# Performance work log

Measured on AMD Instinct MI355X. Metric: run time of the kernel, lower is better.

The kernel has to match this reference:

```python
import jax, jax.numpy as jnp
import numpy as np

N = 100000   # nodes
E = 1600000  # edges
DIM = 64
DIMS = [128, 64, 64, 64]  # [2*DIM] + 3*[DIM]
MAX_DEG = 64
NUM_LAB = 16

def _leaky(x):
    return jnp.where(x >= 0, x, 0.01 * x)

def _bn(x, g, b, eps=1e-5):
    # BatchNorm1d in training mode: per-feature batch mean / biased variance
    m = x.mean(axis=0)
    v = x.var(axis=0)
    return (x - m) * jax.lax.rsqrt(v + eps) * g + b

def setup_inputs() -> dict:
    key = jax.random.key(0)
    ks = jax.random.split(key, 40)
    d = {}
    d["node_deg"] = jax.random.randint(ks[0], (N,), 0, MAX_DEG + 1)
    d["node_lab"] = jax.random.randint(ks[1], (N,), 0, NUM_LAB)
    d["edge_index"] = jax.random.randint(ks[2], (2, E), 0, N)
    d["emb_deg"] = jax.random.normal(ks[3], (MAX_DEG + 1, DIM), jnp.float32) * 0.1
    d["emb_lab"] = jax.random.normal(ks[4], (NUM_LAB, DIM), jnp.float32) * 0.1
    k = 5
    for i, (n1, n2) in enumerate(zip(DIMS[:-1], DIMS[1:])):
        d[f"w{i}"] = jax.random.normal(ks[k], (n2, n1), jnp.float32) / np.sqrt(n1); k += 1
        d[f"b{i}"] = jnp.zeros((n2,), jnp.float32)
        d[f"g{i}"] = jnp.ones((n2,), jnp.float32)
        d[f"be{i}"] = jnp.zeros((n2,), jnp.float32)
    SUMD = sum(DIMS)  # 320
    d["fw1"] = jax.random.normal(ks[k], (DIM, SUMD), jnp.float32) / np.sqrt(SUMD); k += 1
    d["fb1"] = jnp.zeros((DIM,), jnp.float32)
    d["fg"] = jnp.ones((DIM,), jnp.float32)
    d["fbe"] = jnp.zeros((DIM,), jnp.float32)
    d["fw2"] = jax.random.normal(ks[k], (1, DIM), jnp.float32) / np.sqrt(DIM)
    d["fb2"] = jnp.zeros((1,), jnp.float32)
    return d

def reference(node_deg, node_lab, edge_index, emb_deg, emb_lab,
              w0, b0, g0, be0, w1, b1, g1, be1, w2, b2, g2, be2,
              fw1, fb1, fg, fbe, fw2, fb2):
    src, dst = edge_index[0], edge_index[1]
    # input embedding: concat of degree and label embeddings -> [N, 128]
    x0 = jnp.concatenate([emb_deg[node_deg], emb_lab[node_lab]], axis=1)
    z = [x0]
    for (w, b, g, be) in [(w0, b0, g0, be0), (w1, b1, g1, be1), (w2, b2, g2, be2)]:
        x = z[-1]
        # GINConv (eps=0): h = Linear(x + sum_{j in N(i)} x_j)
        agg = jax.ops.segment_sum(x[src], dst, num_segments=N)
        h = (x + agg) @ w.T + b
        z.append(_leaky(_bn(h, g, be)))
    xc = jnp.concatenate(z, axis=1)  # [N, 320]
    h = _leaky(_bn(xc @ fw1.T + fb1, fg, fbe))
    return jax.nn.sigmoid(h @ fw2.T + fb2).squeeze()  # [N]
```

## Files before the change

kernel.cpp:

```cpp
#include <hip/hip_runtime.h>
#include <math.h>

typedef __bf16 bf16;
typedef __attribute__((ext_vector_type(8))) __bf16 bf16x8;
typedef __attribute__((ext_vector_type(4))) float f32x4;

#define NBLK 128
#define NB_MAX 1600

__device__ __forceinline__ void bn_coeffs(const float* st, const float* g,
                                          const float* be, float inv_n, int d,
                                          float& sc, float& sh) {
  float mean = st[d] * inv_n;
  float var = st[64 + d] * inv_n - mean * mean;
  sc = g[d] * rsqrtf(var + 1e-5f);
  sh = be[d] - mean * sc;
}

__global__ __launch_bounds__(256) void bin_hist_kernel(const int* __restrict__ dst,
                                                       int* __restrict__ cnt,
                                                       int E, int ch, int nb) {
  __shared__ int lcnt[NB_MAX];
  int tid = threadIdx.x, blk = blockIdx.x;
  for (int t = tid; t < nb; t += 256) lcnt[t] = 0;
  __syncthreads();
  int base = blk * ch, eend = min(E, base + ch);
  for (int e = base + tid; e < eend; e += 256) atomicAdd(&lcnt[dst[e] >> 6], 1);
  __syncthreads();
  for (int t = tid; t < nb; t += 256) cnt[blk * nb + t] = lcnt[t];
}

__global__ __launch_bounds__(256) void bin_tot_kernel(const int* __restrict__ cnt,
                                                      int* __restrict__ tot, int nb) {
  int b = blockIdx.x * 256 + threadIdx.x;
  if (b >= nb) return;
  int s = 0;
  for (int blk = 0; blk < NBLK; ++blk) s += cnt[blk * nb + b];
  tot[b] = s;
}

__global__ __launch_bounds__(256) void scan_buckets_kernel(const int* __restrict__ tot,
                                                           int* __restrict__ bucketptr, int nb) {
  __shared__ int lds[256];
  int tid = threadIdx.x;
  const int CH = 7;
  int vals[CH];
  int s = 0;
#pragma unroll
  for (int k = 0; k < CH; ++k) {
    int i = tid * CH + k;
    vals[k] = (i < nb) ? tot[i] : 0;
    s += vals[k];
  }
  lds[tid] = s;
  __syncthreads();
  for (int off = 1; off < 256; off <<= 1) {
    int v = (tid >= off) ? lds[tid - off] : 0;
    __syncthreads();
    lds[tid] += v;
    __syncthreads();
  }
  int run = lds[tid] - s;
  if (tid == 0) bucketptr[0] = 0;
#pragma unroll
  for (int k = 0; k < CH; ++k) {
    int i = tid * CH + k;
    run += vals[k];
    if (i < nb) bucketptr[i + 1] = run;
  }
}

__global__ __launch_bounds__(256) void bin_off_kernel(const int* __restrict__ cnt,
                                                      const int* __restrict__ bucketptr,
                                                      int* __restrict__ woff, int nb) {
  int b = blockIdx.x * 256 + threadIdx.x;
  if (b >= nb) return;
  int run = bucketptr[b];
  for (int blk = 0; blk < NBLK; ++blk) {
    woff[blk * nb + b] = run;
    run += cnt[blk * nb + b];
  }
}

__global__ __launch_bounds__(256) void bin_scatter_kernel(const int* __restrict__ src,
                                                          const int* __restrict__ dst,
                                                          const int* __restrict__ woff,
                                                          int* __restrict__ packed,
                                                          int E, int ch, int nb) {
  __shared__ int cur[NB_MAX];
  int tid = threadIdx.x, blk = blockIdx.x;
  for (int t = tid; t < nb; t += 256) cur[t] = woff[blk * nb + t];
  __syncthreads();
  int base = blk * ch, eend = min(E, base + ch);
  for (int e = base + tid; e < eend; e += 256) {
    int d = dst[e], s = src[e];
    int pos = atomicAdd(&cur[d >> 6], 1);
    packed[pos] = ((d & 63) << 17) | s;
  }
}

__global__ __launch_bounds__(256) void csr_finalize_kernel(
    const int* __restrict__ packed, const int* __restrict__ bucketptr,
    int* __restrict__ rowptr, int* __restrict__ colidx, int n, int E) {
  __shared__ int hist[64], offs[64];
  int tid = threadIdx.x, b = blockIdx.x;
  if (tid < 64) hist[tid] = 0;
  __syncthreads();
  int beg = bucketptr[b], end = bucketptr[b + 1];
  for (int e = beg + tid; e < end; e += 256) atomicAdd(&hist[packed[e] >> 17], 1);
  __syncthreads();
  if (tid == 0) {
    int run = 0;
    for (int j = 0; j < 64; ++j) { offs[j] = run; run += hist[j]; }
  }
  __syncthreads();
  if (tid < 64) {
    int idx = b * 64 + tid;
    if (idx < n) rowptr[idx] = beg + offs[tid];
    hist[tid] = offs[tid];
  }
  if (b == 0 && tid == 64) rowptr[n] = E;
  __syncthreads();
  for (int e = beg + tid; e < end; e += 256) {
    int w = packed[e];
    int pos = atomicAdd(&hist[w >> 17], 1);
    colidx[beg + pos] = w & 0x1FFFF;
  }
}

__global__ __launch_bounds__(256) void mfma_gemm0(
    const int* __restrict__ deg, const int* __restrict__ lab,
    const float* __restrict__ ed, const float* __restrict__ el,
    const float* __restrict__ W, bf16* __restrict__ y, int n) {
  __shared__ bf16 As[64][136];
  __shared__ bf16 Bs[64][136];
  int tid = threadIdx.x;
  int nbase = blockIdx.x * 64;
  {
    int r = tid >> 2, c = tid & 3;
    int node = nbase + r;
    union { bf16 hh[32]; uint4 u[4]; } t;
    if (node < n) {
      int idx = (c < 2) ? deg[node] : lab[node];
      const float* srcp = (c < 2) ? (ed + (size_t)idx * 64 + c * 32)
                                  : (el + (size_t)idx * 64 + (c - 2) * 32);
#pragma unroll
      for (int j = 0; j < 8; ++j) {
        float4 f = ((const float4*)srcp)[j];
        t.hh[j * 4 + 0] = (bf16)f.x; t.hh[j * 4 + 1] = (bf16)f.y;
        t.hh[j * 4 + 2] = (bf16)f.z; t.hh[j * 4 + 3] = (bf16)f.w;
      }
    } else {
#pragma unroll
      for (int j = 0; j < 4; ++j) t.u[j] = uint4{0, 0, 0, 0};
    }
#pragma unroll
    for (int j = 0; j < 4; ++j) *(uint4*)&As[r][c * 32 + j * 8] = t.u[j];
    const float4* wp = (const float4*)(W + r * 128 + c * 32);
#pragma unroll
    for (int j = 0; j < 4; ++j) {
      float4 f0 = wp[j * 2], f1 = wp[j * 2 + 1];
      union { bf16 h[8]; uint4 u; } tw;
      tw.h[0] = (bf16)f0.x; tw.h[1] = (bf16)f0.y; tw.h[2] = (bf16)f0.z; tw.h[3] = (bf16)f0.w;
      tw.h[4] = (bf16)f1.x; tw.h[5] = (bf16)f1.y; tw.h[6] = (bf16)f1.z; tw.h[7] = (bf16)f1.w;
      *(uint4*)&Bs[r][c * 32 + j * 8] = tw.u;
    }
  }
  __syncthreads();
  int l = tid & 63, w = tid >> 6, m = l & 15, quad = l >> 4;
  f32x4 acc[4] = {{0.f, 0.f, 0.f, 0.f}, {0.f, 0.f, 0.f, 0.f},
                  {0.f, 0.f, 0.f, 0.f}, {0.f, 0.f, 0.f, 0.f}};
#pragma unroll
  for (int k0 = 0; k0 < 128; k0 += 32) {
    bf16x8 a = *(const bf16x8*)&As[w * 16 + m][k0 + quad * 8];
#pragma unroll
    for (int t = 0; t < 4; ++t) {
      bf16x8 b = *(const bf16x8*)&Bs[t * 16 + m][k0 + quad * 8];
      acc[t] = __builtin_amdgcn_mfma_f32_16x16x32_bf16(a, b, acc[t], 0, 0, 0);
    }
  }
#pragma unroll
  for (int t = 0; t < 4; ++t)
#pragma unroll
    for (int r4 = 0; r4 < 4; ++r4) {
      int node = nbase + w * 16 + quad * 4 + r4;
      if (node < n) y[(size_t)node * 64 + t * 16 + m] = (bf16)acc[t][r4];
    }
}

__global__ __launch_bounds__(256) void mfma_gemm_bn(
    const bf16* __restrict__ hin, const float* __restrict__ st,
    const float* __restrict__ g, const float* __restrict__ be, float inv_n,
    const float* __restrict__ W, bf16* __restrict__ z,
    bf16* __restrict__ y, int n) {
  __shared__ bf16 As[64][72];
  __shared__ bf16 Bs[64][72];
  __shared__ float ssc[64], ssh[64];
  int tid = threadIdx.x;
  int nbase = blockIdx.x * 64;
  if (tid < 64) {
    float sc, sh;
    bn_coeffs(st, g, be, inv_n, tid, sc, sh);
    ssc[tid] = sc; ssh[tid] = sh;
  }
  __syncthreads();
  {
    int r = tid >> 2, c = tid & 3;
    int node = nbase + r;
    union { bf16 h[16]; uint4 u[2]; } t;
    if (node < n) {
      const uint4* p = (const uint4*)(hin + (size_t)node * 64 + c * 16);
      union { uint4 u; bf16 h[8]; } a0, a1;
      a0.u = p[0]; a1.u = p[1];
#pragma unroll
      for (int j = 0; j < 8; ++j) {
        int d = c * 16 + j;
        float v = (float)a0.h[j] * ssc[d] + ssh[d];
        v = (v >= 0.f) ? v : 0.01f * v;
        t.h[j] = (bf16)v;
      }
#pragma unroll
      for (int j = 0; j < 8; ++j) {
        int d = c * 16 + 8 + j;
        float v = (float)a1.h[j] * ssc[d] + ssh[d];
        v = (v >= 0.f) ? v : 0.01f * v;
        t.h[8 + j] = (bf16)v;
      }
      *(uint4*)(z + (size_t)node * 64 + c * 16) = t.u[0];
      *(uint4*)(z + (size_t)node * 64 + c * 16 + 8) = t.u[1];
    } else {
      t.u[0] = uint4{0, 0, 0, 0}; t.u[1] = uint4{0, 0, 0, 0};
    }
    *(uint4*)&As[r][c * 16] = t.u[0];
    *(uint4*)&As[r][c * 16 + 8] = t.u[1];
    const float4* wp = (const float4*)(W + r * 64 + c * 16);
#pragma unroll
    for (int j = 0; j < 2; ++j) {
      float4 f0 = wp[j * 2], f1 = wp[j * 2 + 1];
      union { bf16 h[8]; uint4 u; } tw;
      tw.h[0] = (bf16)f0.x; tw.h[1] = (bf16)f0.y; tw.h[2] = (bf16)f0.z; tw.h[3] = (bf16)f0.w;
      tw.h[4] = (bf16)f1.x; tw.h[5] = (bf16)f1.y; tw.h[6] = (bf16)f1.z; tw.h[7] = (bf16)f1.w;
      *(uint4*)&Bs[r][c * 16 + j * 8] = tw.u;
    }
  }
  __syncthreads();
  int l = tid & 63, w = tid >> 6, m = l & 15, quad = l >> 4;
  f32x4 acc[4] = {{0.f, 0.f, 0.f, 0.f}, {0.f, 0.f, 0.f, 0.f},
                  {0.f, 0.f, 0.f, 0.f}, {0.f, 0.f, 0.f, 0.f}};
#pragma unroll
  for (int k0 = 0; k0 < 64; k0 += 32) {
    bf16x8 a = *(const bf16x8*)&As[w * 16 + m][k0 + quad * 8];
#pragma unroll
    for (int t = 0; t < 4; ++t) {
      bf16x8 b = *(const bf16x8*)&Bs[t * 16 + m][k0 + quad * 8];
      acc[t] = __builtin_amdgcn_mfma_f32_16x16x32_bf16(a, b, acc[t], 0, 0, 0);
    }
  }
#pragma unroll
  for (int t = 0; t < 4; ++t)
#pragma unroll
    for (int r4 = 0; r4 < 4; ++r4) {
      int node = nbase + w * 16 + quad * 4 + r4;
      if (node < n) y[(size_t)node * 64 + t * 16 + m] = (bf16)acc[t][r4];
    }
}

__global__ __launch_bounds__(256) void gather_kernel(
    const bf16* __restrict__ y, const int* __restrict__ rowptr,
    const int* __restrict__ colidx, const float* __restrict__ bias,
    bf16* __restrict__ h, float* __restrict__ stats, int n) {
  __shared__ float s_sum[64], s_sq[64];
  int tid = threadIdx.x;
  if (tid < 64) { s_sum[tid] = 0.f; s_sq[tid] = 0.f; }
  __syncthreads();
  int lane = tid & 63, wv = tid >> 6;
  int half = lane >> 5;
  int lh = lane & 31;
  const unsigned* y32 = (const unsigned*)y;
  unsigned* h32 = (unsigned*)h;
  float b0 = bias[2 * lh], b1 = bias[2 * lh + 1];
  float p0 = 0, p1 = 0, q0 = 0, q1 = 0;
  int stride = gridDim.x * 8;
  for (int nodeA = blockIdx.x * 8 + wv * 2; nodeA < n; nodeA += stride) {
    int nodeB = nodeA + 1;
    bool hasB = nodeB < n;
    float a0 = 0, a1 = 0, c0 = 0, c1 = 0;
    int e0 = rowptr[nodeA], f0 = rowptr[nodeA + 1];
    int e1 = hasB ? rowptr[nodeB] : 0;
    int f1 = hasB ? rowptr[nodeB + 1] : 0;
    while (e0 + 8 <= f0 && e1 + 8 <= f1) {
#pragma unroll
      for (int k = 0; k < 4; ++k) {
        int sA = colidx[e0 + 2 * k + half];
        int sB = colidx[e1 + 2 * k + half];
        unsigned dA = y32[(size_t)sA * 32 + lh];
        unsigned dB = y32[(size_t)sB * 32 + lh];
        union { unsigned u; float f; } t0, t1, t2, t3;
        t0.u = dA << 16; t1.u = dA & 0xFFFF0000u;
        t2.u = dB << 16; t3.u = dB & 0xFFFF0000u;
        a0 += t0.f; a1 += t1.f; c0 += t2.f; c1 += t3.f;
      }
      e0 += 8; e1 += 8;
    }
    for (; e0 + 8 <= f0; e0 += 8) {
#pragma unroll
      for (int k = 0; k < 4; ++k) {
        int s = colidx[e0 + 2 * k + half];
        unsigned d = y32[(size_t)s * 32 + lh];
        union { unsigned u; float f; } t0, t1;
        t0.u = d << 16; t1.u = d & 0xFFFF0000u;
        a0 += t0.f; a1 += t1.f;
      }
    }
    for (; e0 + 2 <= f0; e0 += 2) {
      int s = colidx[e0 + half];
      unsigned d = y32[(size_t)s * 32 + lh];
      union { unsigned u; float f; } t0, t1;
      t0.u = d << 16; t1.u = d & 0xFFFF0000u;
      a0 += t0.f; a1 += t1.f;
    }
    if (e0 < f0) {
      int s = colidx[e0];
      unsigned d = y32[(size_t)s * 32 + lh];
      if (half == 0) {
        union { unsigned u; float f; } t0, t1;
        t0.u = d << 16; t1.u = d & 0xFFFF0000u;
        a0 += t0.f; a1 += t1.f;
      }
    }
    for (; e1 + 8 <= f1; e1 += 8) {
#pragma unroll
      for (int k = 0; k < 4; ++k) {
        int s = colidx[e1 + 2 * k + half];
        unsigned d = y32[(size_t)s * 32 + lh];
        union { unsigned u; float f; } t0, t1;
        t0.u = d << 16; t1.u = d & 0xFFFF0000u;
        c0 += t0.f; c1 += t1.f;
      }
    }
    for (; e1 + 2 <= f1; e1 += 2) {
      int s = colidx[e1 + half];
      unsigned d = y32[(size_t)s * 32 + lh];
      union { unsigned u; float f; } t0, t1;
      t0.u = d << 16; t1.u = d & 0xFFFF0000u;
      c0 += t0.f; c1 += t1.f;
    }
    if (e1 < f1) {
      int s = colidx[e1];
      unsigned d = y32[(size_t)s * 32 + lh];
      if (half == 0) {
        union { unsigned u; float f; } t0, t1;
        t0.u = d << 16; t1.u = d & 0xFFFF0000u;
        c0 += t0.f; c1 += t1.f;
      }
    }
    a0 += __shfl_xor(a0, 32); a1 += __shfl_xor(a1, 32);
    c0 += __shfl_xor(c0, 32); c1 += __shfl_xor(c1, 32);
    int node = half ? nodeB : nodeA;
    float u0 = half ? c0 : a0;
    float u1 = half ? c1 : a1;
    if (half == 0 || hasB) {
      unsigned sd = y32[(size_t)node * 32 + lh];
      union { unsigned u; float f; } s0, s1;
      s0.u = sd << 16; s1.u = sd & 0xFFFF0000u;
      float v0 = u0 + s0.f + b0;
      float v1 = u1 + s1.f + b1;
      union { bf16 hh[2]; unsigned u; } o;
      o.hh[0] = (bf16)v0; o.hh[1] = (bf16)v1;
      h32[(size_t)node * 32 + lh] = o.u;
      p0 += v0; q0 += v0 * v0;
      p1 += v1; q1 += v1 * v1;
    }
  }
  atomicAdd(&s_sum[2 * lh], p0); atomicAdd(&s_sq[2 * lh], q0);
  atomicAdd(&s_sum[2 * lh + 1], p1); atomicAdd(&s_sq[2 * lh + 1], q1);
  __syncthreads();
  if (tid < 64) {
    atomicAdd(&stats[tid], s_sum[tid]);
    atomicAdd(&stats[64 + tid], s_sq[tid]);
  }
}

__global__ __launch_bounds__(256) void mfma_final(
    const int* __restrict__ deg, const int* __restrict__ lab,
    const float* __restrict__ ed, const float* __restrict__ el,
    const bf16* __restrict__ z1, const bf16* __restrict__ z2,
    const bf16* __restrict__ h2, const float* __restrict__ st2,
    const float* __restrict__ g2, const float* __restrict__ be2, float inv_n,
    const float* __restrict__ fw1, const float* __restrict__ fb1,
    bf16* __restrict__ hf, float* __restrict__ stats, int n) {
  __shared__ bf16 As[64][136];
  __shared__ bf16 Bs[64][136];
  __shared__ float s_sum[64], s_sq[64], ssc[64], ssh[64];
  int tid = threadIdx.x;
  if (tid < 64) {
    s_sum[tid] = 0.f; s_sq[tid] = 0.f;
    float sc, sh;
    bn_coeffs(st2, g2, be2, inv_n, tid, sc, sh);
    ssc[tid] = sc; ssh[tid] = sh;
  }
  int nbase = blockIdx.x * 64;
  int l = tid & 63, w = tid >> 6, m = l & 15, quad = l >> 4;
  int r = tid >> 2, c = tid & 3;
  int node_r = nbase + r;
  f32x4 acc[4] = {{0.f, 0.f, 0.f, 0.f}, {0.f, 0.f, 0.f, 0.f},
                  {0.f, 0.f, 0.f, 0.f}, {0.f, 0.f, 0.f, 0.f}};

#pragma unroll
  for (int seg = 0; seg < 4; ++seg) {
    __syncthreads();
    if (seg == 0) {
      union { bf16 hh[32]; uint4 u[4]; } t;
      if (node_r < n) {
        int idx = (c < 2) ? deg[node_r] : lab[node_r];
        const float* srcp = (c < 2) ? (ed + (size_t)idx * 64 + c * 32)
                                    : (el + (size_t)idx * 64 + (c - 2) * 32);
#pragma unroll
        for (int j = 0; j < 8; ++j) {
          float4 f = ((const float4*)srcp)[j];
          t.hh[j * 4 + 0] = (bf16)f.x; t.hh[j * 4 + 1] = (bf16)f.y;
          t.hh[j * 4 + 2] = (bf16)f.z; t.hh[j * 4 + 3] = (bf16)f.w;
        }
      } else {
#pragma unroll
        for (int j = 0; j < 4; ++j) t.u[j] = uint4{0, 0, 0, 0};
      }
#pragma unroll
      for (int j = 0; j < 4; ++j) *(uint4*)&As[r][c * 32 + j * 8] = t.u[j];
      const float4* wp = (const float4*)(fw1 + r * 320 + c * 32);
#pragma unroll
      for (int j = 0; j < 4; ++j) {
        float4 f0 = wp[j * 2], f1 = wp[j * 2 + 1];
        union { bf16 h[8]; uint4 u; } tw;
        tw.h[0] = (bf16)f0.x; tw.h[1] = (bf16)f0.y; tw.h[2] = (bf16)f0.z; tw.h[3] = (bf16)f0.w;
        tw.h[4] = (bf16)f1.x; tw.h[5] = (bf16)f1.y; tw.h[6] = (bf16)f1.z; tw.h[7] = (bf16)f1.w;
        *(uint4*)&Bs[r][c * 32 + j * 8] = tw.u;
      }
    } else if (seg < 3) {
      const bf16* zz = (seg == 1) ? z1 : z2;
      uint4 v[2] = {};
      if (node_r < n) {
        const uint4* p = (const uint4*)(zz + (size_t)node_r * 64 + c * 16);
        v[0] = p[0]; v[1] = p[1];
      }
      *(uint4*)&As[r][c * 16] = v[0];
      *(uint4*)&As[r][c * 16 + 8] = v[1];
      const float4* wp = (const float4*)(fw1 + r * 320 + (seg == 1 ? 128 : 192) + c * 16);
#pragma unroll
      for (int j = 0; j < 2; ++j) {
        float4 f0 = wp[j * 2], f1 = wp[j * 2 + 1];
        union { bf16 h[8]; uint4 u; } t;
        t.h[0] = (bf16)f0.x; t.h[1] = (bf16)f0.y; t.h[2] = (bf16)f0.z; t.h[3] = (bf16)f0.w;
        t.h[4] = (bf16)f1.x; t.h[5] = (bf16)f1.y; t.h[6] = (bf16)f1.z; t.h[7] = (bf16)f1.w;
        *(uint4*)&Bs[r][c * 16 + j * 8] = t.u;
      }
    } else {
      union { bf16 h[16]; uint4 u[2]; } t;
      if (node_r < n) {
        const uint4* p = (const uint4*)(h2 + (size_t)node_r * 64 + c * 16);
        union { uint4 u; bf16 h[8]; } a0, a1;
        a0.u = p[0]; a1.u = p[1];
#pragma unroll
        for (int j = 0; j < 8; ++j) {
          int d = c * 16 + j;
          float v = (float)a0.h[j] * ssc[d] + ssh[d];
          v = (v >= 0.f) ? v : 0.01f * v;
          t.h[j] = (bf16)v;
        }
#pragma unroll
        for (int j = 0; j < 8; ++j) {
          int d = c * 16 + 8 + j;
          float v = (float)a1.h[j] * ssc[d] + ssh[d];
          v = (v >= 0.f) ? v : 0.01f * v;
          t.h[8 + j] = (bf16)v;
        }
      } else {
        t.u[0] = uint4{0, 0, 0, 0}; t.u[1] = uint4{0, 0, 0, 0};
      }
      *(uint4*)&As[r][c * 16] = t.u[0];
      *(uint4*)&As[r][c * 16 + 8] = t.u[1];
      const float4* wp = (const float4*)(fw1 + r * 320 + 256 + c * 16);
#pragma unroll
      for (int j = 0; j < 2; ++j) {
        float4 f0 = wp[j * 2], f1 = wp[j * 2 + 1];
        union { bf16 h[8]; uint4 u; } tw;
        tw.h[0] = (bf16)f0.x; tw.h[1] = (bf16)f0.y; tw.h[2] = (bf16)f0.z; tw.h[3] = (bf16)f0.w;
        tw.h[4] = (bf16)f1.x; tw.h[5] = (bf16)f1.y; tw.h[6] = (bf16)f1.z; tw.h[7] = (bf16)f1.w;
        *(uint4*)&Bs[r][c * 16 + j * 8] = tw.u;
      }
    }
    __syncthreads();
    int kmax = (seg == 0) ? 128 : 64;
    for (int k0 = 0; k0 < kmax; k0 += 32) {
      bf16x8 a = *(const bf16x8*)&As[w * 16 + m][k0 + quad * 8];
#pragma unroll
      for (int t = 0; t < 4; ++t) {
        bf16x8 b = *(const bf16x8*)&Bs[t * 16 + m][k0 + quad * 8];
        acc[t] = __builtin_amdgcn_mfma_f32_16x16x32_bf16(a, b, acc[t], 0, 0, 0);
      }
    }
  }

#pragma unroll
  for (int t = 0; t < 4; ++t) {
    int o = t * 16 + m;
    float bv = fb1[o];
    float s = 0.f, q = 0.f;
#pragma unroll
    for (int r4 = 0; r4 < 4; ++r4) {
      int node = nbase + w * 16 + quad * 4 + r4;
      if (node < n) {
        float v = acc[t][r4] + bv;
        hf[(size_t)node * 64 + o] = (bf16)v;
        s += v;
        q += v * v;
      }
    }
    atomicAdd(&s_sum[o], s);
    atomicAdd(&s_sq[o], q);
  }
  __syncthreads();
  if (tid < 64) {
    atomicAdd(&stats[tid], s_sum[tid]);
    atomicAdd(&stats[64 + tid], s_sq[tid]);
  }
}

__global__ __launch_bounds__(256) void final_out_kernel(
    const bf16* __restrict__ hf, const float* __restrict__ st,
    const float* __restrict__ g, const float* __restrict__ be, float inv_n,
    const float* __restrict__ fw2, const float* __restrict__ fb2,
    float* __restrict__ out, int n) {
  int lane = threadIdx.x & 63;
  int node = blockIdx.x * 4 + (threadIdx.x >> 6);
  if (node >= n) return;
  float sc, sh;
  bn_coeffs(st, g, be, inv_n, lane, sc, sh);
  float v = (float)hf[(size_t)node * 64 + lane] * sc + sh;
  v = (v >= 0.f) ? v : 0.01f * v;
  v *= fw2[lane];
#pragma unroll
  for (int off = 32; off > 0; off >>= 1) v += __shfl_xor(v, off);
  if (lane == 0) out[node] = 1.f / (1.f + expf(-(v + fb2[0])));
}

extern "C" void kernel_launch(void* const* d_in, const int* in_sizes, int n_in,
                              void* d_out, int out_size, void* d_ws, size_t ws_size,
                              hipStream_t stream) {
  const int* node_deg = (const int*)d_in[0];
  const int* node_lab = (const int*)d_in[1];
  const int* ei = (const int*)d_in[2];
  const float* emb_deg = (const float*)d_in[3];
  const float* emb_lab = (const float*)d_in[4];
  const float* w0 = (const float*)d_in[5];
  const float* b0 = (const float*)d_in[6];
  const float* g0 = (const float*)d_in[7];
  const float* be0 = (const float*)d_in[8];
  const float* w1 = (const float*)d_in[9];
  const float* b1 = (const float*)d_in[10];
  const float* g1 = (const float*)d_in[11];
  const float* be1 = (const float*)d_in[12];
  const float* w2 = (const float*)d_in[13];
  const float* b2 = (const float*)d_in[14];
  const float* g2 = (const float*)d_in[15];
  const float* be2 = (const float*)d_in[16];
  const float* fw1 = (const float*)d_in[17];
  const float* fb1 = (const float*)d_in[18];
  const float* fg = (const float*)d_in[19];
  const float* fbe = (const float*)d_in[20];
  const float* fw2 = (const float*)d_in[21];
  const float* fb2 = (const float*)d_in[22];

  const int N = in_sizes[0];
  const int E = in_sizes[2] / 2;
  const int* src = ei;
  const int* dst = ei + E;
  const int NB = (N + 63) >> 6;
  const int CH = (E + NBLK - 1) / NBLK;
  const float inv_n = 1.0f / N;

  char* ws = (char*)d_ws;
  size_t off = 0;
  auto alloc = [&](size_t bytes) {
    void* p = ws + off;
    off += (bytes + 255) & ~(size_t)255;
    return p;
  };
  bf16* z1 = (bf16*)alloc((size_t)N * 64 * 2);
  bf16* z2 = (bf16*)alloc((size_t)N * 64 * 2);
  bf16* h = (bf16*)alloc((size_t)N * 64 * 2);
  bf16* y = (bf16*)alloc((size_t)N * 64 * 2);
  int* packed = (int*)alloc((size_t)E * 4);
  int* colidx = (int*)alloc((size_t)E * 4);
  int* rowptr = (int*)alloc((size_t)(N + 1) * 4);
  int* cnt = (int*)alloc((size_t)NBLK * NB * 4);
  int* woff = (int*)alloc((size_t)NBLK * NB * 4);
  int* btot = (int*)alloc((size_t)NB * 4);
  int* bucketptr = (int*)alloc((size_t)(NB + 1) * 4);
  float* stats = (float*)alloc(4 * 256 * 4);

  hipMemsetAsync(stats, 0, 4 * 256 * 4, stream);

  bin_hist_kernel<<<NBLK, 256, 0, stream>>>(dst, cnt, E, CH, NB);
  bin_tot_kernel<<<(NB + 255) / 256, 256, 0, stream>>>(cnt, btot, NB);
  scan_buckets_kernel<<<1, 256, 0, stream>>>(btot, bucketptr, NB);
  bin_off_kernel<<<(NB + 255) / 256, 256, 0, stream>>>(cnt, bucketptr, woff, NB);
  bin_scatter_kernel<<<NBLK, 256, 0, stream>>>(src, dst, woff, packed, E, CH, NB);
  csr_finalize_kernel<<<NB, 256, 0, stream>>>(packed, bucketptr, rowptr, colidx, N, E);

  int ngrid = (N + 63) / 64;
  int ggrid = 2048;

  mfma_gemm0<<<ngrid, 256, 0, stream>>>(node_deg, node_lab, emb_deg, emb_lab, w0, y, N);
  gather_kernel<<<ggrid, 256, 0, stream>>>(y, rowptr, colidx, b0, h, stats, N);
  mfma_gemm_bn<<<ngrid, 256, 0, stream>>>(h, stats, g0, be0, inv_n, w1, z1, y, N);
  gather_kernel<<<ggrid, 256, 0, stream>>>(y, rowptr, colidx, b1, h, stats + 256, N);
  mfma_gemm_bn<<<ngrid, 256, 0, stream>>>(h, stats + 256, g1, be1, inv_n, w2, z2, y, N);
  gather_kernel<<<ggrid, 256, 0, stream>>>(y, rowptr, colidx, b2, h, stats + 512, N);
  mfma_final<<<ngrid, 256, 0, stream>>>(node_deg, node_lab, emb_deg, emb_lab, z1, z2, h,
                                        stats + 512, g2, be2, inv_n, fw1, fb1, y,
                                        stats + 768, N);
  final_out_kernel<<<(N + 3) / 4, 256, 0, stream>>>(y, stats + 768, fg, fbe, inv_n,
                                                    fw2, fb2, (float*)d_out, N);
}
```

Baseline: 547.6 us.

## Partition CSR neighbors by source-node quarter and gather in grid-synchronized phases

The CSR build now sorts each node's neighbor list by which quarter of the node range the source falls in, and records per-node split offsets. The gather kernel is rewritten to make four passes, one per source quarter, with a spin-wait grid barrier between them so every block reads from the same quarter of y at once. Partial sums are kept in shared memory, and bias, the self term and the BN statistics are applied at the end. The aim is to keep the gathered rows in L2 and reduce random HBM traffic. In exchange the kernel relies on a grid barrier that assumes all 2000 blocks are resident at once (with a capped spin as the fallback), adds barrier overhead, and does more shuffle work per edge.

```diff
diff --git a/kernel.cpp b/kernel.cpp
--- a/kernel.cpp
+++ b/kernel.cpp
@@ -7,6 +7,7 @@
 
 #define NBLK 128
 #define NB_MAX 1600
+#define NPB 50
 
 __device__ __forceinline__ void bn_coeffs(const float* st, const float* g,
                                           const float* be, float inv_n, int d,
@@ -101,30 +102,43 @@
 
 __global__ __launch_bounds__(256) void csr_finalize_kernel(
     const int* __restrict__ packed, const int* __restrict__ bucketptr,
-    int* __restrict__ rowptr, int* __restrict__ colidx, int n, int E) {
-  __shared__ int hist[64], offs[64];
+    int* __restrict__ rowptr, int* __restrict__ colidx, int* __restrict__ splits,
+    int n, int E, int TN) {
+  __shared__ int hist[256], offs[256];
   int tid = threadIdx.x, b = blockIdx.x;
-  if (tid < 64) hist[tid] = 0;
+  hist[tid] = 0;
   __syncthreads();
   int beg = bucketptr[b], end = bucketptr[b + 1];
-  for (int e = beg + tid; e < end; e += 256) atomicAdd(&hist[packed[e] >> 17], 1);
+  for (int e = beg + tid; e < end; e += 256) {
+    int w = packed[e];
+    int s = w & 0x1FFFF;
+    int tile = (s >= TN) + (s >= 2 * TN) + (s >= 3 * TN);
+    atomicAdd(&hist[((w >> 17) << 2) + tile], 1);
+  }
   __syncthreads();
   if (tid == 0) {
     int run = 0;
-    for (int j = 0; j < 64; ++j) { offs[j] = run; run += hist[j]; }
-  }
-  __syncthreads();
+    for (int j = 0; j < 256; ++j) { offs[j] = run; run += hist[j]; }
+  }
+  __syncthreads();
+  {
+    int node = b * 64 + (tid >> 2);
+    if (node < n) splits[(size_t)node * 4 + (tid & 3)] = beg + offs[tid];
+  }
   if (tid < 64) {
     int idx = b * 64 + tid;
-    if (idx < n) rowptr[idx] = beg + offs[tid];
-    hist[tid] = offs[tid];
+    if (idx < n) rowptr[idx] = beg + offs[tid << 2];
   }
   if (b == 0 && tid == 64) rowptr[n] = E;
+  __syncthreads();
+  hist[tid] = offs[tid];
   __syncthreads();
   for (int e = beg + tid; e < end; e += 256) {
     int w = packed[e];
-    int pos = atomicAdd(&hist[w >> 17], 1);
-    colidx[beg + pos] = w & 0x1FFFF;
+    int s = w & 0x1FFFF;
+    int tile = (s >= TN) + (s >= 2 * TN) + (s >= 3 * TN);
+    int pos = atomicAdd(&hist[((w >> 17) << 2) + tile], 1);
+    colidx[beg + pos] = s;
   }
 }
 
@@ -265,115 +279,107 @@
     }
 }
 
-__global__ __launch_bounds__(256) void gather_kernel(
+__global__ __launch_bounds__(256, 8) void gather_tiled(
     const bf16* __restrict__ y, const int* __restrict__ rowptr,
-    const int* __restrict__ colidx, const float* __restrict__ bias,
-    bf16* __restrict__ h, float* __restrict__ stats, int n) {
+    const int* __restrict__ splits, const int* __restrict__ colidx,
+    const float* __restrict__ bias, bf16* __restrict__ h,
+    float* __restrict__ stats, int* __restrict__ bar, int n) {
+  __shared__ float accs[NPB][64];
   __shared__ float s_sum[64], s_sq[64];
   int tid = threadIdx.x;
+  int lane = tid & 63, wv = tid >> 6;
+  int g = lane >> 4;
+  int sl = lane & 15;
+  int nb0 = blockIdx.x * NPB;
+  int nb1 = min(n, nb0 + NPB);
+  for (int t = tid; t < NPB * 64; t += 256) ((float*)accs)[t] = 0.f;
   if (tid < 64) { s_sum[tid] = 0.f; s_sq[tid] = 0.f; }
   __syncthreads();
-  int lane = tid & 63, wv = tid >> 6;
-  int half = lane >> 5;
-  int lh = lane & 31;
-  const unsigned* y32 = (const unsigned*)y;
-  unsigned* h32 = (unsigned*)h;
-  float b0 = bias[2 * lh], b1 = bias[2 * lh + 1];
-  float p0 = 0, p1 = 0, q0 = 0, q1 = 0;
-  int stride = gridDim.x * 8;
-  for (int nodeA = blockIdx.x * 8 + wv * 2; nodeA < n; nodeA += stride) {
-    int nodeB = nodeA + 1;
-    bool hasB = nodeB < n;
-    float a0 = 0, a1 = 0, c0 = 0, c1 = 0;
-    int e0 = rowptr[nodeA], f0 = rowptr[nodeA + 1];
-    int e1 = hasB ? rowptr[nodeB] : 0;
-    int f1 = hasB ? rowptr[nodeB + 1] : 0;
-    while (e0 + 8 <= f0 && e1 + 8 <= f1) {
-#pragma unroll
-      for (int k = 0; k < 4; ++k) {
-        int sA = colidx[e0 + 2 * k + half];
-        int sB = colidx[e1 + 2 * k + half];
-        unsigned dA = y32[(size_t)sA * 32 + lh];
-        unsigned dB = y32[(size_t)sB * 32 + lh];
-        union { unsigned u; float f; } t0, t1, t2, t3;
-        t0.u = dA << 16; t1.u = dA & 0xFFFF0000u;
-        t2.u = dB << 16; t3.u = dB & 0xFFFF0000u;
-        a0 += t0.f; a1 += t1.f; c0 += t2.f; c1 += t3.f;
-      }
-      e0 += 8; e1 += 8;
-    }
-    for (; e0 + 8 <= f0; e0 += 8) {
-#pragma unroll
-      for (int k = 0; k < 4; ++k) {
-        int s = colidx[e0 + 2 * k + half];
-        unsigned d = y32[(size_t)s * 32 + lh];
-        union { unsigned u; float f; } t0, t1;
-        t0.u = d << 16; t1.u = d & 0xFFFF0000u;
-        a0 += t0.f; a1 += t1.f;
-      }
-    }
-    for (; e0 + 2 <= f0; e0 += 2) {
-      int s = colidx[e0 + half];
-      unsigned d = y32[(size_t)s * 32 + lh];
-      union { unsigned u; float f; } t0, t1;
-      t0.u = d << 16; t1.u = d & 0xFFFF0000u;
-      a0 += t0.f; a1 += t1.f;
-    }
-    if (e0 < f0) {
-      int s = colidx[e0];
-      unsigned d = y32[(size_t)s * 32 + lh];
-      if (half == 0) {
-        union { unsigned u; float f; } t0, t1;
-        t0.u = d << 16; t1.u = d & 0xFFFF0000u;
-        a0 += t0.f; a1 += t1.f;
-      }
-    }
-    for (; e1 + 8 <= f1; e1 += 8) {
-#pragma unroll
-      for (int k = 0; k < 4; ++k) {
-        int s = colidx[e1 + 2 * k + half];
-        unsigned d = y32[(size_t)s * 32 + lh];
-        union { unsigned u; float f; } t0, t1;
-        t0.u = d << 16; t1.u = d & 0xFFFF0000u;
-        c0 += t0.f; c1 += t1.f;
-      }
-    }
-    for (; e1 + 2 <= f1; e1 += 2) {
-      int s = colidx[e1 + half];
-      unsigned d = y32[(size_t)s * 32 + lh];
-      union { unsigned u; float f; } t0, t1;
-      t0.u = d << 16; t1.u = d & 0xFFFF0000u;
-      c0 += t0.f; c1 += t1.f;
-    }
-    if (e1 < f1) {
-      int s = colidx[e1];
-      unsigned d = y32[(size_t)s * 32 + lh];
-      if (half == 0) {
-        union { unsigned u; float f; } t0, t1;
-        t0.u = d << 16; t1.u = d & 0xFFFF0000u;
-        c0 += t0.f; c1 += t1.f;
-      }
-    }
-    a0 += __shfl_xor(a0, 32); a1 += __shfl_xor(a1, 32);
-    c0 += __shfl_xor(c0, 32); c1 += __shfl_xor(c1, 32);
-    int node = half ? nodeB : nodeA;
-    float u0 = half ? c0 : a0;
-    float u1 = half ? c1 : a1;
-    if (half == 0 || hasB) {
-      unsigned sd = y32[(size_t)node * 32 + lh];
-      union { unsigned u; float f; } s0, s1;
-      s0.u = sd << 16; s1.u = sd & 0xFFFF0000u;
-      float v0 = u0 + s0.f + b0;
-      float v1 = u1 + s1.f + b1;
-      union { bf16 hh[2]; unsigned u; } o;
-      o.hh[0] = (bf16)v0; o.hh[1] = (bf16)v1;
-      h32[(size_t)node * 32 + lh] = o.u;
-      p0 += v0; q0 += v0 * v0;
-      p1 += v1; q1 += v1 * v1;
-    }
-  }
-  atomicAdd(&s_sum[2 * lh], p0); atomicAdd(&s_sq[2 * lh], q0);
-  atomicAdd(&s_sum[2 * lh + 1], p1); atomicAdd(&s_sq[2 * lh + 1], q1);
+  const uint2* y2 = (const uint2*)y;
+
+#pragma unroll 1
+  for (int k = 0; k < 4; ++k) {
+    for (int p0 = nb0 + wv * 2; p0 < nb1; p0 += 8) {
+      bool hasB = (p0 + 1) < nb1;
+      int begA = splits[(size_t)p0 * 4 + k];
+      int endA = (k == 3) ? rowptr[p0 + 1] : splits[(size_t)p0 * 4 + k + 1];
+      int begB = 0, endB = 0;
+      if (hasB) {
+        begB = splits[(size_t)(p0 + 1) * 4 + k];
+        endB = (k == 3) ? rowptr[p0 + 2] : splits[(size_t)(p0 + 1) * 4 + k + 1];
+      }
+      float aA0 = 0, aA1 = 0, aA2 = 0, aA3 = 0;
+      float aB0 = 0, aB1 = 0, aB2 = 0, aB3 = 0;
+      for (int e0 = begA, e1 = begB; e0 < endA || e1 < endB; e0 += 64, e1 += 64) {
+        int cA = endA - e0; if (cA > 64) cA = 64;
+        int cB = endB - e1; if (cB > 64) cB = 64;
+        int csA = (lane < cA) ? colidx[e0 + lane] : 0;
+        int csB = (lane < cB) ? colidx[e1 + lane] : 0;
+        for (int i = 0; i < cA; i += 4) {
+          int idx = i + g;
+          int s = __shfl(csA, idx);
+          uint2 d; d.x = 0u; d.y = 0u;
+          if (idx < cA) d = y2[(size_t)s * 16 + sl];
+          union { unsigned u; float f; } t;
+          t.u = d.x << 16;         aA0 += t.f;
+          t.u = d.x & 0xFFFF0000u; aA1 += t.f;
+          t.u = d.y << 16;         aA2 += t.f;
+          t.u = d.y & 0xFFFF0000u; aA3 += t.f;
+        }
+        for (int i = 0; i < cB; i += 4) {
+          int idx = i + g;
+          int s = __shfl(csB, idx);
+          uint2 d; d.x = 0u; d.y = 0u;
+          if (idx < cB) d = y2[(size_t)s * 16 + sl];
+          union { unsigned u; float f; } t;
+          t.u = d.x << 16;         aB0 += t.f;
+          t.u = d.x & 0xFFFF0000u; aB1 += t.f;
+          t.u = d.y << 16;         aB2 += t.f;
+          t.u = d.y & 0xFFFF0000u; aB3 += t.f;
+        }
+      }
+      aA0 += __shfl_xor(aA0, 16); aA0 += __shfl_xor(aA0, 32);
+      aA1 += __shfl_xor(aA1, 16); aA1 += __shfl_xor(aA1, 32);
+      aA2 += __shfl_xor(aA2, 16); aA2 += __shfl_xor(aA2, 32);
+      aA3 += __shfl_xor(aA3, 16); aA3 += __shfl_xor(aA3, 32);
+      aB0 += __shfl_xor(aB0, 16); aB0 += __shfl_xor(aB0, 32);
+      aB1 += __shfl_xor(aB1, 16); aB1 += __shfl_xor(aB1, 32);
+      aB2 += __shfl_xor(aB2, 16); aB2 += __shfl_xor(aB2, 32);
+      aB3 += __shfl_xor(aB3, 16); aB3 += __shfl_xor(aB3, 32);
+      if (lane < 16) {
+        float* ra = &accs[p0 - nb0][sl * 4];
+        ra[0] += aA0; ra[1] += aA1; ra[2] += aA2; ra[3] += aA3;
+        if (hasB) {
+          float* rb = &accs[p0 + 1 - nb0][sl * 4];
+          rb[0] += aB0; rb[1] += aB1; rb[2] += aB2; rb[3] += aB3;
+        }
+      }
+    }
+    if (k < 3) {
+      __syncthreads();
+      if (tid == 0) {
+        __hip_atomic_fetch_add(&bar[k], 1, __ATOMIC_RELAXED, __HIP_MEMORY_SCOPE_AGENT);
+        int spin = 0;
+        while (__hip_atomic_load(&bar[k], __ATOMIC_RELAXED, __HIP_MEMORY_SCOPE_AGENT) <
+                   (int)gridDim.x && ++spin < 20000)
+          __builtin_amdgcn_s_sleep(2);
+      }
+      __syncthreads();
+    }
+  }
+  __syncthreads();
+  int d = tid & 63;
+  float bv = bias[d];
+  float p = 0.f, q = 0.f;
+  int nd = (nb1 - nb0) * 64;
+  for (int idx = tid; idx < nd; idx += 256) {
+    int node = nb0 + (idx >> 6);
+    float v = ((const float*)accs)[idx] + (float)y[(size_t)node * 64 + d] + bv;
+    h[(size_t)node * 64 + d] = (bf16)v;
+    p += v; q += v * v;
+  }
+  atomicAdd(&s_sum[d], p);
+  atomicAdd(&s_sq[d], q);
   __syncthreads();
   if (tid < 64) {
     atomicAdd(&stats[tid], s_sum[tid]);
@@ -578,6 +584,7 @@
   const int NB = (N + 63) >> 6;
   const int CH = (E + NBLK - 1) / NBLK;
   const float inv_n = 1.0f / N;
+  const int TN = (N + 3) / 4;
 
   char* ws = (char*)d_ws;
   size_t off = 0;
@@ -593,30 +600,35 @@
   int* packed = (int*)alloc((size_t)E * 4);
   int* colidx = (int*)alloc((size_t)E * 4);
   int* rowptr = (int*)alloc((size_t)(N + 1) * 4);
+  int* splits = (int*)alloc((size_t)N * 4 * 4);
   int* cnt = (int*)alloc((size_t)NBLK * NB * 4);
   int* woff = (int*)alloc((size_t)NBLK * NB * 4);
   int* btot = (int*)alloc((size_t)NB * 4);
   int* bucketptr = (int*)alloc((size_t)(NB + 1) * 4);
-  float* stats = (float*)alloc(4 * 256 * 4);
-
-  hipMemsetAsync(stats, 0, 4 * 256 * 4, stream);
+  float* stats = (float*)alloc(4 * 256 * 4 + 64);
+  int* bar = (int*)(stats + 4 * 256);
+
+  hipMemsetAsync(stats, 0, 4 * 256 * 4 + 64, stream);
 
   bin_hist_kernel<<<NBLK, 256, 0, stream>>>(dst, cnt, E, CH, NB);
   bin_tot_kernel<<<(NB + 255) / 256, 256, 0, stream>>>(cnt, btot, NB);
   scan_buckets_kernel<<<1, 256, 0, stream>>>(btot, bucketptr, NB);
   bin_off_kernel<<<(NB + 255) / 256, 256, 0, stream>>>(cnt, bucketptr, woff, NB);
   bin_scatter_kernel<<<NBLK, 256, 0, stream>>>(src, dst, woff, packed, E, CH, NB);
-  csr_finalize_kernel<<<NB, 256, 0, stream>>>(packed, bucketptr, rowptr, colidx, N, E);
+  csr_finalize_kernel<<<NB, 256, 0, stream>>>(packed, bucketptr, rowptr, colidx, splits,
+                                              N, E, TN);
 
   int ngrid = (N + 63) / 64;
-  int ggrid = 2048;
+  int gblk = (N + NPB - 1) / NPB;
 
   mfma_gemm0<<<ngrid, 256, 0, stream>>>(node_deg, node_lab, emb_deg, emb_lab, w0, y, N);
-  gather_kernel<<<ggrid, 256, 0, stream>>>(y, rowptr, colidx, b0, h, stats, N);
+  gather_tiled<<<gblk, 256, 0, stream>>>(y, rowptr, splits, colidx, b0, h, stats, bar, N);
   mfma_gemm_bn<<<ngrid, 256, 0, stream>>>(h, stats, g0, be0, inv_n, w1, z1, y, N);
-  gather_kernel<<<ggrid, 256, 0, stream>>>(y, rowptr, colidx, b1, h, stats + 256, N);
+  gather_tiled<<<gblk, 256, 0, stream>>>(y, rowptr, splits, colidx, b1, h, stats + 256,
+                                         bar + 4, N);
   mfma_gemm_bn<<<ngrid, 256, 0, stream>>>(h, stats + 256, g1, be1, inv_n, w2, z2, y, N);
-  gather_kernel<<<ggrid, 256, 0, stream>>>(y, rowptr, colidx, b2, h, stats + 512, N);
+  gather_tiled<<<gblk, 256, 0, stream>>>(y, rowptr, splits, colidx, b2, h, stats + 512,
+                                         bar + 8, N);
   mfma_final<<<ngrid, 256, 0, stream>>>(node_deg, node_lab, emb_deg, emb_lab, z1, z2, h,
                                         stats + 512, g2, be2, inv_n, fw1, fb1, y,
                                         stats + 768, N);
```

Measured after the change: 1.731 ms. 3.16x slower.

## Restructure gather to 8 nodes per wave with 16-byte row loads

Applied to the files above, without the earlier changes.

The CSR gather kernel now gives each wave 8 nodes, with 8 lanes per node each loading a 16-byte chunk (8 bf16 features) per neighbour row. Previously each wave handled 2 nodes with 32-bit loads split across half-waves. Edge loops are unrolled by 8 with ballot-based wave-uniform exits, and an occupancy hint is added to the launch bounds. The grid is resized to cover the node count with a cap. The aim is fewer, wider memory transactions and more independent loads in flight. The costs are higher register pressure and divergence when nodes in the same wave have unequal degrees.

```diff
diff --git a/kernel.cpp b/kernel.cpp
--- a/kernel.cpp
+++ b/kernel.cpp
@@ -265,7 +265,7 @@
     }
 }
 
-__global__ __launch_bounds__(256) void gather_kernel(
+__global__ __launch_bounds__(256, 6) void gather_kernel(
     const bf16* __restrict__ y, const int* __restrict__ rowptr,
     const int* __restrict__ colidx, const float* __restrict__ bias,
     bf16* __restrict__ h, float* __restrict__ stats, int n) {
@@ -274,106 +274,109 @@
   if (tid < 64) { s_sum[tid] = 0.f; s_sq[tid] = 0.f; }
   __syncthreads();
   int lane = tid & 63, wv = tid >> 6;
-  int half = lane >> 5;
-  int lh = lane & 31;
-  const unsigned* y32 = (const unsigned*)y;
-  unsigned* h32 = (unsigned*)h;
-  float b0 = bias[2 * lh], b1 = bias[2 * lh + 1];
-  float p0 = 0, p1 = 0, q0 = 0, q1 = 0;
-  int stride = gridDim.x * 8;
-  for (int nodeA = blockIdx.x * 8 + wv * 2; nodeA < n; nodeA += stride) {
-    int nodeB = nodeA + 1;
-    bool hasB = nodeB < n;
-    float a0 = 0, a1 = 0, c0 = 0, c1 = 0;
-    int e0 = rowptr[nodeA], f0 = rowptr[nodeA + 1];
-    int e1 = hasB ? rowptr[nodeB] : 0;
-    int f1 = hasB ? rowptr[nodeB + 1] : 0;
-    while (e0 + 8 <= f0 && e1 + 8 <= f1) {
-#pragma unroll
-      for (int k = 0; k < 4; ++k) {
-        int sA = colidx[e0 + 2 * k + half];
-        int sB = colidx[e1 + 2 * k + half];
-        unsigned dA = y32[(size_t)sA * 32 + lh];
-        unsigned dB = y32[(size_t)sB * 32 + lh];
-        union { unsigned u; float f; } t0, t1, t2, t3;
-        t0.u = dA << 16; t1.u = dA & 0xFFFF0000u;
-        t2.u = dB << 16; t3.u = dB & 0xFFFF0000u;
-        a0 += t0.f; a1 += t1.f; c0 += t2.f; c1 += t3.f;
-      }
-      e0 += 8; e1 += 8;
-    }
-    for (; e0 + 8 <= f0; e0 += 8) {
-#pragma unroll
-      for (int k = 0; k < 4; ++k) {
-        int s = colidx[e0 + 2 * k + half];
-        unsigned d = y32[(size_t)s * 32 + lh];
-        union { unsigned u; float f; } t0, t1;
-        t0.u = d << 16; t1.u = d & 0xFFFF0000u;
-        a0 += t0.f; a1 += t1.f;
-      }
-    }
-    for (; e0 + 2 <= f0; e0 += 2) {
-      int s = colidx[e0 + half];
-      unsigned d = y32[(size_t)s * 32 + lh];
-      union { unsigned u; float f; } t0, t1;
-      t0.u = d << 16; t1.u = d & 0xFFFF0000u;
-      a0 += t0.f; a1 += t1.f;
-    }
-    if (e0 < f0) {
-      int s = colidx[e0];
-      unsigned d = y32[(size_t)s * 32 + lh];
-      if (half == 0) {
-        union { unsigned u; float f; } t0, t1;
-        t0.u = d << 16; t1.u = d & 0xFFFF0000u;
-        a0 += t0.f; a1 += t1.f;
-      }
-    }
-    for (; e1 + 8 <= f1; e1 += 8) {
-#pragma unroll
-      for (int k = 0; k < 4; ++k) {
-        int s = colidx[e1 + 2 * k + half];
-        unsigned d = y32[(size_t)s * 32 + lh];
-        union { unsigned u; float f; } t0, t1;
-        t0.u = d << 16; t1.u = d & 0xFFFF0000u;
-        c0 += t0.f; c1 += t1.f;
-      }
-    }
-    for (; e1 + 2 <= f1; e1 += 2) {
-      int s = colidx[e1 + half];
-      unsigned d = y32[(size_t)s * 32 + lh];
-      union { unsigned u; float f; } t0, t1;
-      t0.u = d << 16; t1.u = d & 0xFFFF0000u;
-      c0 += t0.f; c1 += t1.f;
-    }
-    if (e1 < f1) {
-      int s = colidx[e1];
-      unsigned d = y32[(size_t)s * 32 + lh];
-      if (half == 0) {
-        union { unsigned u; float f; } t0, t1;
-        t0.u = d << 16; t1.u = d & 0xFFFF0000u;
-        c0 += t0.f; c1 += t1.f;
-      }
-    }
-    a0 += __shfl_xor(a0, 32); a1 += __shfl_xor(a1, 32);
-    c0 += __shfl_xor(c0, 32); c1 += __shfl_xor(c1, 32);
-    int node = half ? nodeB : nodeA;
-    float u0 = half ? c0 : a0;
-    float u1 = half ? c1 : a1;
-    if (half == 0 || hasB) {
-      unsigned sd = y32[(size_t)node * 32 + lh];
-      union { unsigned u; float f; } s0, s1;
-      s0.u = sd << 16; s1.u = sd & 0xFFFF0000u;
-      float v0 = u0 + s0.f + b0;
-      float v1 = u1 + s1.f + b1;
-      union { bf16 hh[2]; unsigned u; } o;
-      o.hh[0] = (bf16)v0; o.hh[1] = (bf16)v1;
-      h32[(size_t)node * 32 + lh] = o.u;
-      p0 += v0; q0 += v0 * v0;
-      p1 += v1; q1 += v1 * v1;
-    }
-  }
-  atomicAdd(&s_sum[2 * lh], p0); atomicAdd(&s_sq[2 * lh], q0);
-  atomicAdd(&s_sum[2 * lh + 1], p1); atomicAdd(&s_sq[2 * lh + 1], q1);
+  int g = lane >> 3, lh = lane & 7;
+  const uint4* y4 = (const uint4*)y;
+  uint4* h4 = (uint4*)h;
+  float bj[8];
+#pragma unroll
+  for (int j = 0; j < 8; ++j) bj[j] = bias[8 * lh + j];
+  float p[8] = {0.f, 0.f, 0.f, 0.f, 0.f, 0.f, 0.f, 0.f};
+  float q[8] = {0.f, 0.f, 0.f, 0.f, 0.f, 0.f, 0.f, 0.f};
+  int stride = gridDim.x * 32;
+
+#define ACC8(d)                                                      \
+  {                                                                  \
+    union { unsigned u; float f; } t_;                               \
+    t_.u = (d).x << 16;         acc[0] += t_.f;                      \
+    t_.u = (d).x & 0xFFFF0000u; acc[1] += t_.f;                      \
+    t_.u = (d).y << 16;         acc[2] += t_.f;                      \
+    t_.u = (d).y & 0xFFFF0000u; acc[3] += t_.f;                      \
+    t_.u = (d).z << 16;         acc[4] += t_.f;                      \
+    t_.u = (d).z & 0xFFFF0000u; acc[5] += t_.f;                      \
+    t_.u = (d).w << 16;         acc[6] += t_.f;                      \
+    t_.u = (d).w & 0xFFFF0000u; acc[7] += t_.f;                      \
+  }
+
+  for (int nb = (blockIdx.x * 4 + wv) * 8; nb < n; nb += stride) {
+    int node = nb + g;
+    bool valid = node < n;
+    int e = valid ? rowptr[node] : 0;
+    int f = valid ? rowptr[node + 1] : 0;
+    float acc[8] = {0.f, 0.f, 0.f, 0.f, 0.f, 0.f, 0.f, 0.f};
+    for (;;) {
+      bool a = (e + 8 <= f);
+      if (__ballot(a) == 0ull) break;
+      if (a) {
+        int s0 = colidx[e + 0], s1 = colidx[e + 1], s2 = colidx[e + 2], s3 = colidx[e + 3];
+        int s4 = colidx[e + 4], s5 = colidx[e + 5], s6 = colidx[e + 6], s7 = colidx[e + 7];
+        uint4 d0 = y4[(size_t)s0 * 8 + lh];
+        uint4 d1 = y4[(size_t)s1 * 8 + lh];
+        uint4 d2 = y4[(size_t)s2 * 8 + lh];
+        uint4 d3 = y4[(size_t)s3 * 8 + lh];
+        uint4 d4 = y4[(size_t)s4 * 8 + lh];
+        uint4 d5 = y4[(size_t)s5 * 8 + lh];
+        uint4 d6 = y4[(size_t)s6 * 8 + lh];
+        uint4 d7 = y4[(size_t)s7 * 8 + lh];
+        ACC8(d0); ACC8(d1); ACC8(d2); ACC8(d3);
+        ACC8(d4); ACC8(d5); ACC8(d6); ACC8(d7);
+        e += 8;
+      }
+    }
+    {
+      bool a = (e + 4 <= f);
+      if (__ballot(a) != 0ull) {
+        if (a) {
+          int s0 = colidx[e + 0], s1 = colidx[e + 1], s2 = colidx[e + 2], s3 = colidx[e + 3];
+          uint4 d0 = y4[(size_t)s0 * 8 + lh];
+          uint4 d1 = y4[(size_t)s1 * 8 + lh];
+          uint4 d2 = y4[(size_t)s2 * 8 + lh];
+          uint4 d3 = y4[(size_t)s3 * 8 + lh];
+          ACC8(d0); ACC8(d1); ACC8(d2); ACC8(d3);
+          e += 4;
+        }
+      }
+    }
+#pragma unroll
+    for (int t = 0; t < 3; ++t) {
+      bool a = e < f;
+      if (a) {
+        int s = colidx[e];
+        uint4 d = y4[(size_t)s * 8 + lh];
+        ACC8(d);
+        ++e;
+      }
+    }
+    if (valid) {
+      uint4 sd = y4[(size_t)node * 8 + lh];
+      float sv[8];
+      {
+        union { unsigned u; float f; } t_;
+        t_.u = sd.x << 16;         sv[0] = t_.f;
+        t_.u = sd.x & 0xFFFF0000u; sv[1] = t_.f;
+        t_.u = sd.y << 16;         sv[2] = t_.f;
+        t_.u = sd.y & 0xFFFF0000u; sv[3] = t_.f;
+        t_.u = sd.z << 16;         sv[4] = t_.f;
+        t_.u = sd.z & 0xFFFF0000u; sv[5] = t_.f;
+        t_.u = sd.w << 16;         sv[6] = t_.f;
+        t_.u = sd.w & 0xFFFF0000u; sv[7] = t_.f;
+      }
+      union { bf16 hh[8]; uint4 u; } o;
+#pragma unroll
+      for (int j = 0; j < 8; ++j) {
+        float v = acc[j] + sv[j] + bj[j];
+        o.hh[j] = (bf16)v;
+        p[j] += v;
+        q[j] += v * v;
+      }
+      h4[(size_t)node * 8 + lh] = o.u;
+    }
+  }
+#undef ACC8
+#pragma unroll
+  for (int j = 0; j < 8; ++j) {
+    atomicAdd(&s_sum[8 * lh + j], p[j]);
+    atomicAdd(&s_sq[8 * lh + j], q[j]);
+  }
   __syncthreads();
   if (tid < 64) {
     atomicAdd(&stats[tid], s_sum[tid]);
@@ -609,7 +612,9 @@
   csr_finalize_kernel<<<NB, 256, 0, stream>>>(packed, bucketptr, rowptr, colidx, N, E);
 
   int ngrid = (N + 63) / 64;
-  int ggrid = 2048;
+  int ggrid = (N + 127) / 128;
+  if (ggrid > 2048) ggrid = 2048;
+  if (ggrid < 1) ggrid = 1;
 
   mfma_gemm0<<<ngrid, 256, 0, stream>>>(node_deg, node_lab, emb_deg, emb_lab, w0, y, N);
   gather_kernel<<<ggrid, 256, 0, stream>>>(y, rowptr, colidx, b0, h, stats, N);
```

Measured after the change: 521.6 us (median of 2 runs). -4.8%, faster.
